# Optimization experiments

Measured on AMD Instinct MI355X. Metric: run time of the kernel, lower is better.

Reference implementation:

```python
import jax, jax.numpy as jnp
import numpy as np

C = 128          # num_channels
HID = 256        # mlp hidden = 2*C
HEAD_DIM = 16    # C // num_heads (8)
SCALE = 1.0 / np.sqrt(HEAD_DIM)
EPS = 1e-5


def _linear_init(key, fan_in, fan_out):
    kw, kb = jax.random.split(key)
    s = 1.0 / np.sqrt(fan_in)
    w = jax.random.uniform(kw, (fan_in, fan_out), minval=-s, maxval=s, dtype=jnp.float32)
    b = jax.random.uniform(kb, (fan_out,), minval=-s, maxval=s, dtype=jnp.float32)
    return w, b


def setup_inputs() -> dict:
    key = jax.random.key(0)
    ks = jax.random.split(key, 8)
    x = jax.random.normal(ks[0], (4, C, 64, 64), dtype=jnp.float32)
    wq, bq = _linear_init(ks[1], C, C)
    wk, bk = _linear_init(ks[2], C, C)
    wv, bv = _linear_init(ks[3], C, C)
    wo, bo = _linear_init(ks[4], C, C)
    w1, b1 = _linear_init(ks[5], C, HID)
    w2, b2 = _linear_init(ks[6], HID, C)
    return {
        "x": x,
        "ln1_w": jnp.ones((C,), jnp.float32), "ln1_b": jnp.zeros((C,), jnp.float32),
        "wq": wq, "bq": bq, "wk": wk, "bk": bk, "wv": wv, "bv": bv,
        "wo": wo, "bo": bo,
        "ln2_w": jnp.ones((C,), jnp.float32), "ln2_b": jnp.zeros((C,), jnp.float32),
        "w1": w1, "b1": b1, "w2": w2, "b2": b2,
    }


def _layernorm(x, w, b):
    mu = jnp.mean(x, axis=-1, keepdims=True)
    var = jnp.mean(jnp.square(x - mu), axis=-1, keepdims=True)
    return (x - mu) * jax.lax.rsqrt(var + EPS) * w + b


def reference(x, ln1_w, ln1_b, wq, bq, wk, bk, wv, bv, wo, bo, ln2_w, ln2_b, w1, b1, w2, b2):
    B, Cc, H, W = x.shape
    t = x.reshape(B, Cc, H * W).transpose(0, 2, 1)  # [B, S, C]
    xl = _layernorm(t, ln1_w, ln1_b)
    q = xl @ wq + bq
    k = xl @ wk + bk
    v = xl @ wv + bv
    scores = jnp.einsum('bqc,bkc->bqk', q, k) * SCALE  # [B, S, S]
    # Faithful to source: softmax over dim=1 (the QUERY axis).
    attn = jax.nn.softmax(scores, axis=1)
    att_out = jnp.einsum('bqk,bkc->bqc', attn, v) @ wo + bo
    t = att_out + t
    m = _layernorm(t, ln2_w, ln2_b) @ w1 + b1
    m = jax.nn.gelu(m, approximate=False) @ w2 + b2
    t = jax.nn.gelu(m, approximate=False) + t  # second GELU per source
    return t.transpose(0, 2, 1).reshape(B, Cc, H, W)
```

## Files before the change

### kernel.cpp

```cpp
#include <hip/hip_runtime.h>
#include <math.h>

#define S 4096
#define CNUM 128
#define BATCH 4
#define MTOT (BATCH * S)
#define SCLOG2E 0.36067376022224085f
#define EPSLN 1e-5f
#define KSPLIT 4
#define QSPLIT 4

typedef __attribute__((ext_vector_type(8))) short bf16x8;
typedef __attribute__((ext_vector_type(4))) float f32x4;

__device__ __forceinline__ float gelu_exact(float x) {
    return 0.5f * x * (1.0f + erff(x * 0.7071067811865476f));
}

__device__ __forceinline__ unsigned short f2b(float f) {
    union { float f; unsigned int u; } v; v.f = f;
    unsigned int r = (v.u + 0x7FFFu + ((v.u >> 16) & 1u)) >> 16;
    return (unsigned short)r;
}
__device__ __forceinline__ unsigned short f2b_ru(float f) {
    return (unsigned short)((__float_as_uint(f) + 0x8000u) >> 16);
}
__device__ __forceinline__ float b2f(unsigned short u) {
    return __uint_as_float((unsigned)u << 16);
}

__device__ __forceinline__ void gl_lds16(const void* g, void* l) {
    __builtin_amdgcn_global_load_lds(
        (__attribute__((address_space(1))) void*)g,
        (__attribute__((address_space(3))) void*)l, 16, 0, 0);
}

__global__ __launch_bounds__(256) void ln1_transpose(
    const float* __restrict__ x, const float* __restrict__ w, const float* __restrict__ bb,
    unsigned short* __restrict__ xlh, float* __restrict__ t)
{
    __shared__ float tile[128][65];
    __shared__ float mu[64], rs[64];
    const int b = blockIdx.y;
    const int s0 = blockIdx.x * 64;
    const float* xb = x + (size_t)b * CNUM * S;
    for (int i = threadIdx.x; i < 128 * 64; i += 256) {
        int c = i >> 6, sl = i & 63;
        tile[c][sl] = xb[(size_t)c * S + s0 + sl];
    }
    __syncthreads();
    if (threadIdx.x < 64) {
        float sum = 0.f, sq = 0.f;
        for (int c = 0; c < 128; ++c) {
            float v = tile[c][threadIdx.x];
            sum += v; sq += v * v;
        }
        float m = sum * (1.f / 128.f);
        float var = sq * (1.f / 128.f) - m * m;
        mu[threadIdx.x] = m;
        rs[threadIdx.x] = rsqrtf(var + EPSLN);
    }
    __syncthreads();
    for (int i = threadIdx.x; i < 128 * 64; i += 256) {
        int c = i & 127, sl = i >> 7;
        float v = tile[c][sl];
        size_t idx = ((size_t)b * S + s0 + sl) * CNUM + c;
        t[idx] = v;
        xlh[idx] = f2b((v - mu[sl]) * rs[sl] * w[c] + bb[c]);
    }
}

__global__ __launch_bounds__(256) void convw(
    const float* __restrict__ wq, const float* __restrict__ wk, const float* __restrict__ wv,
    const float* __restrict__ wo, const float* __restrict__ w1, const float* __restrict__ w2,
    const float* __restrict__ bq, const float* __restrict__ bk, const float* __restrict__ bv,
    unsigned short* __restrict__ wqkvh, unsigned short* __restrict__ woh,
    unsigned short* __restrict__ w1h, unsigned short* __restrict__ w2h,
    float* __restrict__ bqkv)
{
    int a = blockIdx.y;
    int idx = blockIdx.x * 256 + threadIdx.x;
    if (a == 6) {
        if (idx < 128) bqkv[idx] = bq[idx];
        else if (idx < 256) bqkv[idx] = bk[idx - 128];
        else if (idx < 384) bqkv[idx] = bv[idx - 256];
        return;
    }
    const float* src; unsigned short* dst; int Nsh, Ksz;
    switch (a) {
        case 0: src = wq; dst = wqkvh;          Nsh = 7; Ksz = 128; break;
        case 1: src = wk; dst = wqkvh + 16384;  Nsh = 7; Ksz = 128; break;
        case 2: src = wv; dst = wqkvh + 32768;  Nsh = 7; Ksz = 128; break;
        case 3: src = wo; dst = woh;            Nsh = 7; Ksz = 128; break;
        case 4: src = w1; dst = w1h;            Nsh = 8; Ksz = 128; break;
        default: src = w2; dst = w2h;           Nsh = 7; Ksz = 256; break;
    }
    int total = Ksz << Nsh;
    if (idx >= total) return;
    int k = idx >> Nsh, n = idx & ((1 << Nsh) - 1);
    dst[n * Ksz + k] = f2b(src[idx]);
}

template<int KT>
__global__ __launch_bounds__(256) void gemm_mfma(
    const unsigned short* __restrict__ A, const unsigned short* __restrict__ Bt,
    const float* __restrict__ bias, const float* __restrict__ res,
    void* __restrict__ Cv, int N, int epi)
{
    constexpr int CH = KT / 8;
    constexpr int CSH = (KT == 128) ? 4 : 5;
    __shared__ unsigned short As[64 * KT];
    __shared__ unsigned short Bs[128 * KT];
    const int bm = blockIdx.y * 64;
    const int bn = blockIdx.x * 128;
    const int z = blockIdx.z;
    const unsigned short* Btz = (epi == 7) ? Bt + z * 16384 : Bt;
    const float* biasz = (epi == 7) ? bias + z * 128 : bias;
    const int tid = threadIdx.x;
    const int w = tid >> 6, l = tid & 63;
    const int rw = (w & 1) * 32, cw = (w >> 1) * 64;

    #pragma unroll
    for (int i = 0; i < (64 * CH) / 256; ++i) {
        int cid = i * 256 + tid;
        int r = cid >> CSH, c = cid & (CH - 1);
        int p = (c & ~15) | ((c ^ r) & 15);
        *(ulonglong2*)(As + r * KT + p * 8) =
            *(const ulonglong2*)(A + (size_t)(bm + r) * KT + c * 8);
    }
    #pragma unroll
    for (int i = 0; i < (128 * CH) / 256; ++i) {
        int cid = i * 256 + tid;
        int r = cid >> CSH, c = cid & (CH - 1);
        int p = (c & ~15) | ((c ^ r) & 15);
        *(ulonglong2*)(Bs + r * KT + p * 8) =
            *(const ulonglong2*)(Btz + (size_t)(bn + r) * KT + c * 8);
    }
    __syncthreads();

    f32x4 zero = {0.f, 0.f, 0.f, 0.f};
    f32x4 acc[2][4];
    #pragma unroll
    for (int i = 0; i < 2; ++i)
        #pragma unroll
        for (int j = 0; j < 4; ++j) acc[i][j] = zero;

    #pragma unroll
    for (int ks = 0; ks < KT / 32; ++ks) {
        int c_lin = ks * 4 + (l >> 4);
        bf16x8 a[2], bfr[4];
        #pragma unroll
        for (int i = 0; i < 2; ++i) {
            int m = rw + i * 16 + (l & 15);
            int p = (c_lin & ~15) | ((c_lin ^ m) & 15);
            a[i] = *(const bf16x8*)(As + m * KT + p * 8);
        }
        #pragma unroll
        for (int j = 0; j < 4; ++j) {
            int n = cw + j * 16 + (l & 15);
            int p = (c_lin & ~15) | ((c_lin ^ n) & 15);
            bfr[j] = *(const bf16x8*)(Bs + n * KT + p * 8);
        }
        #pragma unroll
        for (int i = 0; i < 2; ++i)
            #pragma unroll
            for (int j = 0; j < 4; ++j)
                acc[i][j] = __builtin_amdgcn_mfma_f32_16x16x32_bf16(a[i], bfr[j], acc[i][j], 0, 0, 0);
    }

    #pragma unroll
    for (int i = 0; i < 2; ++i) {
        int rowbase = bm + rw + i * 16 + (l >> 4) * 4;
        #pragma unroll
        for (int j = 0; j < 4; ++j) {
            int col = bn + cw + j * 16 + (l & 15);
            float v[4];
            #pragma unroll
            for (int reg = 0; reg < 4; ++reg) v[reg] = acc[i][j][reg] + biasz[col];
            if (epi == 2) {
                #pragma unroll
                for (int reg = 0; reg < 4; ++reg)
                    ((float*)Cv)[(size_t)(rowbase + reg) * N + col] =
                        v[reg] + res[(size_t)(rowbase + reg) * N + col];
            } else if (epi == 6) {
                #pragma unroll
                for (int reg = 0; reg < 4; ++reg)
                    ((unsigned short*)Cv)[(size_t)(rowbase + reg) * N + col] = f2b(gelu_exact(v[reg]));
            } else if (epi == 8) {
                int bb = rowbase >> 12, s = rowbase & 4095;
                float4 o;
                o.x = gelu_exact(v[0]) + res[(size_t)(rowbase + 0) * N + col];
                o.y = gelu_exact(v[1]) + res[(size_t)(rowbase + 1) * N + col];
                o.z = gelu_exact(v[2]) + res[(size_t)(rowbase + 2) * N + col];
                o.w = gelu_exact(v[3]) + res[(size_t)(rowbase + 3) * N + col];
                *(float4*)(((float*)Cv) + ((size_t)(bb * 128 + col)) * 4096 + s) = o;
            } else {
                if (z < 2) {
                    unsigned short* dst = ((unsigned short*)Cv) + (size_t)z * MTOT * 128;
                    #pragma unroll
                    for (int reg = 0; reg < 4; ++reg)
                        dst[(size_t)(rowbase + reg) * 128 + col] = f2b(v[reg]);
                } else {
                    int bb = rowbase >> 12, s = rowbase & 4095;
                    int kc = s >> 6, g = (s >> 3) & 7;
                    ushort4 o;
                    o.x = f2b(v[0]); o.y = f2b(v[1]); o.z = f2b(v[2]); o.w = f2b(v[3]);
                    *(ushort4*)(((unsigned short*)Cv) + (size_t)2 * MTOT * 128 +
                                (((size_t)bb * 64 + kc) << 13) +
                                col * 64 + ((g ^ (col & 7)) << 3) + (s & 7)) = o;
                }
            }
        }
    }
}

__global__ __launch_bounds__(256) void colsum(
    const unsigned short* __restrict__ qh, const unsigned short* __restrict__ kh,
    float* __restrict__ psum_all)
{
    __shared__ unsigned short Qs[128 * 128];
    __shared__ unsigned short Ks[128 * 128];
    __shared__ float csum[2][128];
    const int b = blockIdx.z;
    const unsigned short* Q = qh + (size_t)b * S * 128;
    const unsigned short* Km = kh + (size_t)b * S * 128;
    const int bn = blockIdx.x * 128;
    const int q0 = blockIdx.y * (S / QSPLIT);
    const int tid = threadIdx.x;
    const int w = tid >> 6, l = tid & 63;
    const int wr = (w >> 1) * 64, wc = (w & 1) * 64;
    const int lm = l & 15, lq = l >> 4;

    #pragma unroll
    for (int i = 0; i < 8; ++i) {
        int cid = i * 256 + tid;
        int r = cid >> 4, c = cid & 15;
        int p = c ^ (r & 15);
        *(ulonglong2*)(Ks + r * 128 + p * 8) =
            *(const ulonglong2*)(Km + (size_t)(bn + r) * 128 + c * 8);
    }

    float jsum[4] = {0.f, 0.f, 0.f, 0.f};
    for (int qt = 0; qt < (S / QSPLIT) / 128; ++qt) {
        __syncthreads();
        #pragma unroll
        for (int i = 0; i < 8; ++i) {
            int cid = i * 256 + tid;
            int r = cid >> 4, c = cid & 15;
            int p = c ^ (r & 15);
            *(ulonglong2*)(Qs + r * 128 + p * 8) =
                *(const ulonglong2*)(Q + (size_t)(q0 + qt * 128 + r) * 128 + c * 8);
        }
        __syncthreads();

        f32x4 zero = {0.f, 0.f, 0.f, 0.f};
        f32x4 acc[4][4];
        #pragma unroll
        for (int i = 0; i < 4; ++i)
            #pragma unroll
            for (int j = 0; j < 4; ++j) acc[i][j] = zero;

        #pragma unroll
        for (int ks = 0; ks < 4; ++ks) {
            bf16x8 a[4], bfr[4];
            #pragma unroll
            for (int i = 0; i < 4; ++i) {
                int m = wr + i * 16 + lm;
                int p = (ks * 4 + lq) ^ (m & 15);
                a[i] = *(const bf16x8*)(Qs + m * 128 + p * 8);
            }
            #pragma unroll
            for (int j = 0; j < 4; ++j) {
                int n = wc + j * 16 + lm;
                int p = (ks * 4 + lq) ^ (n & 15);
                bfr[j] = *(const bf16x8*)(Ks + n * 128 + p * 8);
            }
            #pragma unroll
            for (int i = 0; i < 4; ++i)
                #pragma unroll
                for (int j = 0; j < 4; ++j)
                    acc[i][j] = __builtin_amdgcn_mfma_f32_16x16x32_bf16(a[i], bfr[j], acc[i][j], 0, 0, 0);
        }

        #pragma unroll
        for (int i = 0; i < 4; ++i)
            #pragma unroll
            for (int j = 0; j < 4; ++j)
                #pragma unroll
                for (int reg = 0; reg < 4; ++reg)
                    jsum[j] += b2f(f2b_ru(exp2f(acc[i][j][reg] * SCLOG2E)));
    }

    #pragma unroll
    for (int j = 0; j < 4; ++j) {
        jsum[j] += __shfl_xor(jsum[j], 16);
        jsum[j] += __shfl_xor(jsum[j], 32);
    }
    if (l < 16) {
        #pragma unroll
        for (int j = 0; j < 4; ++j)
            csum[w >> 1][wc + j * 16 + l] = jsum[j];
    }
    __syncthreads();
    if (tid < 128)
        psum_all[((size_t)(blockIdx.y * BATCH + b)) * S + bn + tid] = csum[0][tid] + csum[1][tid];
}

__global__ __launch_bounds__(256) void vscale(
    unsigned short* __restrict__ Vimg_all, const float* __restrict__ psum_all)
{
    const int b = blockIdx.z;
    unsigned short* Vimg = Vimg_all + (size_t)b * CNUM * S;
    int i = (blockIdx.x * 256 + threadIdx.x) * 4;
    int kc = i >> 13;
    int off = i & 8191;
    int c = off >> 6;
    int p = (off >> 3) & 7;
    int g = p ^ (c & 7);
    int k = kc * 64 + g * 8 + (off & 7);
    float4 L = *(const float4*)(psum_all + (size_t)b * S + k);
    #pragma unroll
    for (int t = 1; t < QSPLIT; ++t) {
        float4 Lt = *(const float4*)(psum_all + ((size_t)(t * BATCH + b)) * S + k);
        L.x += Lt.x; L.y += Lt.y; L.z += Lt.z; L.w += Lt.w;
    }
    ushort4 v = *(ushort4*)(Vimg + i);
    v.x = f2b(b2f(v.x) / L.x);
    v.y = f2b(b2f(v.y) / L.y);
    v.z = f2b(b2f(v.z) / L.z);
    v.w = f2b(b2f(v.w) / L.w);
    *(ushort4*)(Vimg + i) = v;
}

__global__ __launch_bounds__(256, 2) void fused_attnv(
    const unsigned short* __restrict__ qh, const unsigned short* __restrict__ kh,
    const unsigned short* __restrict__ Vimg_all, unsigned short* __restrict__ parts)
{
    __shared__ unsigned short Ks[64 * 128];
    __shared__ unsigned short Vls[128 * 64];
    __shared__ unsigned short Ps[4][32 * 64];
    const int b = blockIdx.z;
    const unsigned short* Qm = qh + (size_t)b * S * 128;
    const unsigned short* Km = kh + (size_t)b * S * 128;
    const unsigned short* Vimg = Vimg_all + (((size_t)b * 64) << 13);
    unsigned short* Pout = parts + (size_t)blockIdx.x * ((size_t)MTOT * CNUM)
                                 + (size_t)b * S * CNUM;
    const int q0 = blockIdx.y * 128;
    const int kt0 = blockIdx.x * (S / KSPLIT / 64);
    const int tid = threadIdx.x;
    const int w = tid >> 6, l = tid & 63;
    const int lm = l & 15, lq = l >> 4;
    const int row0 = q0 + w * 32;
    unsigned short* Pw = Ps[w];

    bf16x8 aq[2][4];
    #pragma unroll
    for (int i = 0; i < 2; ++i)
        #pragma unroll
        for (int ks = 0; ks < 4; ++ks)
            aq[i][ks] = *(const bf16x8*)(Qm + (size_t)(row0 + i * 16 + lm) * 128 + (ks * 4 + lq) * 8);

    f32x4 zero = {0.f, 0.f, 0.f, 0.f};
    f32x4 acco[2][8];
    #pragma unroll
    for (int i = 0; i < 2; ++i)
        #pragma unroll
        for (int j = 0; j < 8; ++j) acco[i][j] = zero;

    for (int kt = 0; kt < S / KSPLIT / 64; ++kt) {
        const int kb = (kt0 + kt) * 64;
        if (kt) __syncthreads();
        #pragma unroll
        for (int i = 0; i < 4; ++i) {
            int cid = i * 256 + tid;
            int r = cid >> 4, c = cid & 15;
            int p = c ^ (r & 15);
            *(ulonglong2*)(Ks + r * 128 + p * 8) =
                *(const ulonglong2*)(Km + (size_t)(kb + r) * 128 + c * 8);
        }
        {
            const unsigned short* src = Vimg + (((size_t)(kt0 + kt)) << 13) + tid * 8;
            #pragma unroll
            for (int i = 0; i < 4; ++i)
                gl_lds16(src + i * 2048, &Vls[(i * 256 + tid) * 8]);
        }
        __syncthreads();

        f32x4 accs[2][4];
        #pragma unroll
        for (int i = 0; i < 2; ++i)
            #pragma unroll
            for (int j = 0; j < 4; ++j) accs[i][j] = zero;
        #pragma unroll
        for (int ks = 0; ks < 4; ++ks) {
            bf16x8 bk_[4];
            #pragma unroll
            for (int j = 0; j < 4; ++j) {
                int n = j * 16 + lm;
                int p = (ks * 4 + lq) ^ (n & 15);
                bk_[j] = *(const bf16x8*)(Ks + n * 128 + p * 8);
            }
            #pragma unroll
            for (int i = 0; i < 2; ++i)
                #pragma unroll
                for (int j = 0; j < 4; ++j)
                    accs[i][j] = __builtin_amdgcn_mfma_f32_16x16x32_bf16(aq[i][ks], bk_[j], accs[i][j], 0, 0, 0);
        }

        #pragma unroll
        for (int i = 0; i < 2; ++i)
            #pragma unroll
            for (int j = 0; j < 4; ++j)
                #pragma unroll
                for (int reg = 0; reg < 4; ++reg) {
                    int prow = i * 16 + lq * 4 + reg;
                    int pcol = j * 16 + lm;
                    unsigned short h = f2b_ru(exp2f(accs[i][j][reg] * SCLOG2E));
                    int s8 = (prow ^ (prow >> 3)) & 7;
                    Pw[prow * 64 + (((pcol >> 3) ^ s8) << 3) + (pcol & 7)] = h;
                }

        #pragma unroll
        for (int ks = 0; ks < 2; ++ks) {
            bf16x8 ap[2];
            #pragma unroll
            for (int i = 0; i < 2; ++i) {
                int prow = i * 16 + lm;
                int s8 = (prow ^ (prow >> 3)) & 7;
                ap[i] = *(const bf16x8*)(Pw + prow * 64 + (((ks * 4 + lq) ^ s8) << 3));
            }
            #pragma unroll
            for (int j = 0; j < 8; ++j) {
                int n = j * 16 + lm;
                bf16x8 bv = *(const bf16x8*)(Vls + n * 64 + (((ks * 4 + lq) ^ (n & 7)) << 3));
                acco[0][j] = __builtin_amdgcn_mfma_f32_16x16x32_bf16(ap[0], bv, acco[0][j], 0, 0, 0);
                acco[1][j] = __builtin_amdgcn_mfma_f32_16x16x32_bf16(ap[1], bv, acco[1][j], 0, 0, 0);
            }
        }
    }

    #pragma unroll
    for (int i = 0; i < 2; ++i) {
        int rowb = row0 + i * 16 + lq * 4;
        #pragma unroll
        for (int j = 0; j < 8; ++j) {
            int col = j * 16 + lm;
            #pragma unroll
            for (int reg = 0; reg < 4; ++reg)
                Pout[(size_t)(rowb + reg) * CNUM + col] = f2b(acco[i][j][reg]);
        }
    }
}

__global__ __launch_bounds__(256) void reduce8b(
    const ushort4* __restrict__ parts, ushort4* __restrict__ dst)
{
    size_t i = (size_t)blockIdx.x * 256 + threadIdx.x;
    const size_t stride = (size_t)MTOT * CNUM / 4;
    float sx = 0.f, sy = 0.f, sz = 0.f, sw = 0.f;
    #pragma unroll
    for (int p = 0; p < KSPLIT; ++p) {
        ushort4 v = parts[i + p * stride];
        sx += b2f(v.x); sy += b2f(v.y); sz += b2f(v.z); sw += b2f(v.w);
    }
    ushort4 o;
    o.x = f2b(sx); o.y = f2b(sy); o.z = f2b(sz); o.w = f2b(sw);
    dst[i] = o;
}

__global__ __launch_bounds__(256) void ln_rows(
    const float* __restrict__ y, const float* __restrict__ w, const float* __restrict__ bb,
    unsigned short* __restrict__ zh)
{
    int row = blockIdx.x * 4 + (threadIdx.x >> 6);
    int lane = threadIdx.x & 63;
    const float* yr = y + (size_t)row * CNUM;
    float v0 = yr[lane], v1 = yr[lane + 64];
    float sum = v0 + v1, sq = v0 * v0 + v1 * v1;
    #pragma unroll
    for (int off = 32; off; off >>= 1) {
        sum += __shfl_xor(sum, off);
        sq  += __shfl_xor(sq, off);
    }
    float mean = sum * (1.f / 128.f);
    float var = sq * (1.f / 128.f) - mean * mean;
    float r = rsqrtf(var + EPSLN);
    zh[(size_t)row * CNUM + lane]      = f2b((v0 - mean) * r * w[lane] + bb[lane]);
    zh[(size_t)row * CNUM + lane + 64] = f2b((v1 - mean) * r * w[lane + 64] + bb[lane + 64]);
}

extern "C" void kernel_launch(void* const* d_in, const int* in_sizes, int n_in,
                              void* d_out, int out_size, void* d_ws, size_t ws_size,
                              hipStream_t stream)
{
    (void)in_sizes; (void)n_in; (void)out_size; (void)ws_size;
    const float* x    = (const float*)d_in[0];
    const float* ln1w = (const float*)d_in[1];
    const float* ln1b = (const float*)d_in[2];
    const float* wq   = (const float*)d_in[3];
    const float* bq   = (const float*)d_in[4];
    const float* wk   = (const float*)d_in[5];
    const float* bk   = (const float*)d_in[6];
    const float* wv   = (const float*)d_in[7];
    const float* bv   = (const float*)d_in[8];
    const float* wo   = (const float*)d_in[9];
    const float* bo   = (const float*)d_in[10];
    const float* ln2w = (const float*)d_in[11];
    const float* ln2b = (const float*)d_in[12];
    const float* w1   = (const float*)d_in[13];
    const float* b1   = (const float*)d_in[14];
    const float* w2   = (const float*)d_in[15];
    const float* b2   = (const float*)d_in[16];
    float* out = (float*)d_out;

    float* ws = (float*)d_ws;
    const size_t NSC = (size_t)MTOT * CNUM;
    float* t      = ws;
    float* y      = t + NSC;
    float* psum   = y + NSC;
    unsigned short* parts = (unsigned short*)(psum + (size_t)QSPLIT * BATCH * S);
    unsigned short* xlh = parts + (size_t)KSPLIT * NSC;
    unsigned short* qh  = xlh + NSC;
    unsigned short* kh  = qh + NSC;
    unsigned short* Vt  = kh + NSC;
    unsigned short* attouth = Vt + NSC;
    unsigned short* zh  = attouth + NSC;
    unsigned short* hh  = zh + NSC;
    unsigned short* wqkvh = hh + (size_t)MTOT * 256;
    unsigned short* woh = wqkvh + 3 * 16384;
    unsigned short* w1h = woh + 16384;
    unsigned short* w2h = w1h + 32768;
    float* bqkv = (float*)(w2h + 32768);

    ln1_transpose<<<dim3(S / 64, BATCH), 256, 0, stream>>>(x, ln1w, ln1b, xlh, t);
    convw<<<dim3(128, 7), 256, 0, stream>>>(wq, wk, wv, wo, w1, w2, bq, bk, bv,
                                            wqkvh, woh, w1h, w2h, bqkv);

    gemm_mfma<128><<<dim3(1, MTOT / 64, 3), 256, 0, stream>>>(
        xlh, wqkvh, bqkv, nullptr, qh, 128, 7);

    colsum<<<dim3(S / 128, QSPLIT, BATCH), 256, 0, stream>>>(qh, kh, psum);
    vscale<<<dim3(CNUM * S / 4 / 256, 1, BATCH), 256, 0, stream>>>(Vt, psum);
    fused_attnv<<<dim3(KSPLIT, S / 128, BATCH), 256, 0, stream>>>(qh, kh, Vt, parts);
    reduce8b<<<NSC / 4 / 256, 256, 0, stream>>>((const ushort4*)parts, (ushort4*)attouth);

    gemm_mfma<128><<<dim3(1, MTOT / 64), 256, 0, stream>>>(attouth, woh, bo, t, y, 128, 2);
    ln_rows<<<MTOT / 4, 256, 0, stream>>>(y, ln2w, ln2b, zh);
    gemm_mfma<128><<<dim3(2, MTOT / 64), 256, 0, stream>>>(zh, w1h, b1, nullptr, hh, 256, 6);
    gemm_mfma<256><<<dim3(1, MTOT / 64), 256, 0, stream>>>(hh, w2h, b2, y, out, 128, 8);
}
```

Baseline: 244.7 us.

## Shrink attention key tile to 32, double KSPLIT, transpose score MFMA

The fused attention-V kernel now processes 32-key tiles instead of 64. It doubles the key-split factor and raises occupancy to 4 blocks per SM, with LDS shrunk to fit. Scores are computed transposed (K as the A operand), so each lane holds pairs of consecutive keys. These are packed with v_cvt_pk_bf16_f32 and written as 32-bit words into a padded P buffer, removing the scalar 16-bit scattered stores. The changes target LDS store traffic and latency hiding, at the cost of twice as many partial outputs to reduce and more barriers per key.

After: 265.2 us. 8.4% more time.

```diff
diff --git a/kernel.cpp b/kernel.cpp
--- a/kernel.cpp
+++ b/kernel.cpp
@@ -7,11 +7,12 @@
 #define MTOT (BATCH * S)
 #define SCLOG2E 0.36067376022224085f
 #define EPSLN 1e-5f
-#define KSPLIT 4
+#define KSPLIT 8
 #define QSPLIT 4
 
 typedef __attribute__((ext_vector_type(8))) short bf16x8;
 typedef __attribute__((ext_vector_type(4))) float f32x4;
+typedef __attribute__((ext_vector_type(4))) unsigned int u32x4;
 
 __device__ __forceinline__ float gelu_exact(float x) {
     return 0.5f * x * (1.0f + erff(x * 0.7071067811865476f));
@@ -332,13 +333,13 @@
     *(ushort4*)(Vimg + i) = v;
 }
 
-__global__ __launch_bounds__(256, 2) void fused_attnv(
+__global__ __launch_bounds__(256, 4) void fused_attnv(
     const unsigned short* __restrict__ qh, const unsigned short* __restrict__ kh,
     const unsigned short* __restrict__ Vimg_all, unsigned short* __restrict__ parts)
 {
-    __shared__ unsigned short Ks[64 * 128];
+    __shared__ unsigned short Ks[32 * 128];
     __shared__ unsigned short Vls[128 * 64];
-    __shared__ unsigned short Ps[4][32 * 64];
+    __shared__ unsigned int   Ps[128 * 18];
     const int b = blockIdx.z;
     const unsigned short* Qm = qh + (size_t)b * S * 128;
     const unsigned short* Km = kh + (size_t)b * S * 128;
@@ -346,12 +347,13 @@
     unsigned short* Pout = parts + (size_t)blockIdx.x * ((size_t)MTOT * CNUM)
                                  + (size_t)b * S * CNUM;
     const int q0 = blockIdx.y * 128;
-    const int kt0 = blockIdx.x * (S / KSPLIT / 64);
+    const int kb0 = blockIdx.x * (S / KSPLIT);
+    const int kc0 = blockIdx.x * (S / KSPLIT / 64);
     const int tid = threadIdx.x;
     const int w = tid >> 6, l = tid & 63;
     const int lm = l & 15, lq = l >> 4;
     const int row0 = q0 + w * 32;
-    unsigned short* Pw = Ps[w];
+    const int prow0 = w * 32;
 
     bf16x8 aq[2][4];
     #pragma unroll
@@ -367,75 +369,77 @@
         #pragma unroll
         for (int j = 0; j < 8; ++j) acco[i][j] = zero;
 
-    for (int kt = 0; kt < S / KSPLIT / 64; ++kt) {
-        const int kb = (kt0 + kt) * 64;
-        if (kt) __syncthreads();
-        #pragma unroll
-        for (int i = 0; i < 4; ++i) {
-            int cid = i * 256 + tid;
+    for (int kt = 0; kt < S / KSPLIT / 32; ++kt) {
+        const int kb = kb0 + kt * 32;
+        __syncthreads();
+        #pragma unroll
+        for (int i2 = 0; i2 < 2; ++i2) {
+            int cid = i2 * 256 + tid;
             int r = cid >> 4, c = cid & 15;
             int p = c ^ (r & 15);
             *(ulonglong2*)(Ks + r * 128 + p * 8) =
                 *(const ulonglong2*)(Km + (size_t)(kb + r) * 128 + c * 8);
         }
-        {
-            const unsigned short* src = Vimg + (((size_t)(kt0 + kt)) << 13) + tid * 8;
-            #pragma unroll
-            for (int i = 0; i < 4; ++i)
-                gl_lds16(src + i * 2048, &Vls[(i * 256 + tid) * 8]);
+        if ((kt & 1) == 0) {
+            const unsigned short* src = Vimg + ((size_t)(kc0 + (kt >> 1)) << 13) + tid * 8;
+            #pragma unroll
+            for (int i2 = 0; i2 < 4; ++i2)
+                gl_lds16(src + i2 * 2048, &Vls[(i2 * 256 + tid) * 8]);
         }
         __syncthreads();
 
-        f32x4 accs[2][4];
-        #pragma unroll
-        for (int i = 0; i < 2; ++i)
-            #pragma unroll
-            for (int j = 0; j < 4; ++j) accs[i][j] = zero;
+        f32x4 accT[2][2];
+        #pragma unroll
+        for (int ki = 0; ki < 2; ++ki)
+            #pragma unroll
+            for (int qj = 0; qj < 2; ++qj) accT[ki][qj] = zero;
         #pragma unroll
         for (int ks = 0; ks < 4; ++ks) {
-            bf16x8 bk_[4];
-            #pragma unroll
-            for (int j = 0; j < 4; ++j) {
-                int n = j * 16 + lm;
+            bf16x8 kfr[2];
+            #pragma unroll
+            for (int ki = 0; ki < 2; ++ki) {
+                int n = ki * 16 + lm;
                 int p = (ks * 4 + lq) ^ (n & 15);
-                bk_[j] = *(const bf16x8*)(Ks + n * 128 + p * 8);
+                kfr[ki] = *(const bf16x8*)(Ks + n * 128 + p * 8);
             }
             #pragma unroll
-            for (int i = 0; i < 2; ++i)
+            for (int ki = 0; ki < 2; ++ki)
                 #pragma unroll
-                for (int j = 0; j < 4; ++j)
-                    accs[i][j] = __builtin_amdgcn_mfma_f32_16x16x32_bf16(aq[i][ks], bk_[j], accs[i][j], 0, 0, 0);
-        }
-
-        #pragma unroll
-        for (int i = 0; i < 2; ++i)
-            #pragma unroll
-            for (int j = 0; j < 4; ++j)
+                for (int qj = 0; qj < 2; ++qj)
+                    accT[ki][qj] = __builtin_amdgcn_mfma_f32_16x16x32_bf16(kfr[ki], aq[qj][ks], accT[ki][qj], 0, 0, 0);
+        }
+
+        #pragma unroll
+        for (int qj = 0; qj < 2; ++qj) {
+            unsigned int* pw = Ps + (prow0 + qj * 16 + lm) * 18 + lq * 2;
+            #pragma unroll
+            for (int ki = 0; ki < 2; ++ki)
                 #pragma unroll
-                for (int reg = 0; reg < 4; ++reg) {
-                    int prow = i * 16 + lq * 4 + reg;
-                    int pcol = j * 16 + lm;
-                    unsigned short h = f2b_ru(exp2f(accs[i][j][reg] * SCLOG2E));
-                    int s8 = (prow ^ (prow >> 3)) & 7;
-                    Pw[prow * 64 + (((pcol >> 3) ^ s8) << 3) + (pcol & 7)] = h;
+                for (int r2 = 0; r2 < 2; ++r2) {
+                    float e0 = exp2f(accT[ki][qj][2 * r2]     * SCLOG2E);
+                    float e1 = exp2f(accT[ki][qj][2 * r2 + 1] * SCLOG2E);
+                    unsigned int pk;
+                    asm("v_cvt_pk_bf16_f32 %0, %1, %2" : "=v"(pk) : "v"(e0), "v"(e1));
+                    pw[ki * 8 + r2] = pk;
                 }
-
-        #pragma unroll
-        for (int ks = 0; ks < 2; ++ks) {
-            bf16x8 ap[2];
-            #pragma unroll
-            for (int i = 0; i < 2; ++i) {
-                int prow = i * 16 + lm;
-                int s8 = (prow ^ (prow >> 3)) & 7;
-                ap[i] = *(const bf16x8*)(Pw + prow * 64 + (((ks * 4 + lq) ^ s8) << 3));
-            }
-            #pragma unroll
-            for (int j = 0; j < 8; ++j) {
-                int n = j * 16 + lm;
-                bf16x8 bv = *(const bf16x8*)(Vls + n * 64 + (((ks * 4 + lq) ^ (n & 7)) << 3));
-                acco[0][j] = __builtin_amdgcn_mfma_f32_16x16x32_bf16(ap[0], bv, acco[0][j], 0, 0, 0);
-                acco[1][j] = __builtin_amdgcn_mfma_f32_16x16x32_bf16(ap[1], bv, acco[1][j], 0, 0, 0);
-            }
+        }
+
+        bf16x8 ap[2];
+        #pragma unroll
+        for (int i = 0; i < 2; ++i) {
+            const unsigned int* pr = Ps + (prow0 + i * 16 + lm) * 18 + lq * 4;
+            uint2 u0 = *(const uint2*)(pr);
+            uint2 u1 = *(const uint2*)(pr + 2);
+            u32x4 uu = {u0.x, u0.y, u1.x, u1.y};
+            ap[i] = __builtin_bit_cast(bf16x8, uu);
+        }
+        const int vh = (kt & 1) * 4;
+        #pragma unroll
+        for (int j = 0; j < 8; ++j) {
+            int n = j * 16 + lm;
+            bf16x8 bv = *(const bf16x8*)(Vls + n * 64 + (((vh + lq) ^ (n & 7)) << 3));
+            acco[0][j] = __builtin_amdgcn_mfma_f32_16x16x32_bf16(ap[0], bv, acco[0][j], 0, 0, 0);
+            acco[1][j] = __builtin_amdgcn_mfma_f32_16x16x32_bf16(ap[1], bv, acco[1][j], 0, 0, 0);
         }
     }
 
```
